# Optimization experiments

Measured on AMD Instinct MI355X. Metric: run time of the kernel, lower is better.

The kernel has to match this reference:

```python
import jax, jax.numpy as jnp
import numpy as np

B, L, D, N, KEEP, HID = 64, 256, 128, 8192, 64, 1024
IN_DIM = D + KEEP * D + 1  # q + packed subset keys + log_count


def setup_inputs() -> dict:
    key = jax.random.key(0)
    ks = jax.random.split(key, 7)
    q = jax.random.normal(ks[0], (N, D), jnp.float32)
    k = jax.random.normal(ks[1], (B, L, D), jnp.float32)
    batch_idx = jax.random.randint(ks[2], (N,), 0, B)
    mask = jax.random.randint(ks[3], (N, L), 0, 2).astype(bool)
    count = jax.random.randint(ks[4], (N,), 0, L)
    W1 = jax.random.normal(ks[5], (IN_DIM, HID), jnp.float32) / np.sqrt(IN_DIM).astype(np.float32)
    b1 = jnp.zeros((HID,), jnp.float32)
    W2 = jax.random.normal(ks[6], (HID, 1), jnp.float32) / np.sqrt(HID).astype(np.float32)
    b2 = jnp.zeros((1,), jnp.float32)
    return dict(q=q, k=k, batch_idx=batch_idx, mask=mask, count=count,
                W1=W1, b1=b1, W2=W2, b2=b2)


def _pack_subset_keys(k, batch_idx, mask):
    # chain_k: [N, L, D] gather of per-chain key blocks
    chain_k = k[batch_idx]
    pos = jnp.arange(L, dtype=jnp.float32)
    # score = L - pos for masked positions, 0 otherwise -> topk picks first KEEP masked positions
    scores = mask.astype(jnp.float32) * (jnp.float32(L) - pos)[None, :]
    top_scores, top_idx = jax.lax.top_k(scores, KEEP)
    picked = top_scores > 0
    sortable = jnp.where(picked, top_idx, L)  # sentinel L for unpicked
    sortable = jnp.sort(sortable, axis=1)     # restore ascending position order
    picked = sortable < L
    safe_idx = jnp.where(picked, sortable, 0)
    packed = jnp.take_along_axis(chain_k, safe_idx[:, :, None], axis=1)  # [N, KEEP, D]
    packed = packed * picked[:, :, None].astype(packed.dtype)
    return packed.reshape(N, KEEP * D)


def reference(q, k, batch_idx, mask, count, W1, b1, W2, b2):
    packed = _pack_subset_keys(k, batch_idx, mask)
    log_count = jnp.log1p(count.astype(q.dtype))[:, None]
    feat = jnp.concatenate([q, packed, log_count], axis=-1)  # [N, IN_DIM]
    h = jax.nn.gelu(feat @ W1 + b1, approximate=False)       # torch GELU = exact erf
    return (h @ W2 + b2).squeeze(-1)                          # [N]
```

## Files before the change

kernel.cpp:

```cpp
#include <hip/hip_runtime.h>
#include <math.h>

#define N_ROWS 8192
#define B_CH   64
#define L_SEQ  256
#define D_DIM  128
#define KEEP   64
#define HID    1024
#define KTOT   8320
#define KTILES 260
#define HTILES 64

#define KOFF   (N_ROWS * D_DIM)
#define ZOFF   (KOFF + B_CH * L_SEQ * D_DIM)
#define BUF_ELEMS (ZOFF + 128)

#define PACK_BLOCKS 256
#define QK_BLOCKS   1537
#define W1T_BLOCKS  2080
#define PREP_GRID   (PACK_BLOCKS + QK_BLOCKS + W1T_BLOCKS)

typedef unsigned short ushort_t;
typedef __attribute__((ext_vector_type(8))) short  short8;
typedef __attribute__((ext_vector_type(4))) float  float4v;

__device__ __forceinline__ ushort_t f2bf(float f) {
    union { float f; unsigned int u; } v; v.f = f;
    unsigned int u = v.u;
    unsigned int r = u + 0x7fffu + ((u >> 16) & 1u);
    return (ushort_t)(r >> 16);
}

__device__ __forceinline__ void glds16(const void* g, void* l) {
    __builtin_amdgcn_global_load_lds(
        (const __attribute__((address_space(1))) unsigned int*)g,
        (__attribute__((address_space(3))) unsigned int*)l,
        16, 0, 0);
}

__global__ void prep(const float* __restrict__ q, const float* __restrict__ k,
                     const float* __restrict__ W1, const int* __restrict__ mask,
                     const int* __restrict__ batch_idx, const int* __restrict__ count,
                     const float* __restrict__ b2,
                     ushort_t* __restrict__ buf, ushort_t* __restrict__ w1f,
                     int* __restrict__ srcLUT, float* __restrict__ logc,
                     float* __restrict__ out) {
    __shared__ __align__(16) char smem[16640];
    const int blk = blockIdx.x;
    const int t = threadIdx.x;

    if (blk < PACK_BLOCKS) {
        const int n0 = blk * 32;
        int* sidx = (int*)smem;
        int* bidx_l = (int*)(smem + 32 * 65 * 4);
        for (int i = t; i < 32 * 65; i += 256) sidx[i] = -1;
        if (t < 32) {
            int n = n0 + t;
            bidx_l[t] = batch_idx[n];
            logc[n] = log1pf((float)count[n]);
            srcLUT[n] = n * D_DIM;
            out[n] = b2[0];
        }
        __syncthreads();
        const int w = t >> 6, l = t & 63;
        const unsigned long long ltm = (1ull << l) - 1ull;
        for (int r = 0; r < 8; ++r) {
            const int lr = w * 8 + r;
            const int* mrow = mask + (size_t)(n0 + lr) * L_SEQ;
            int m0 = mrow[l] != 0;
            int m1 = mrow[64 + l] != 0;
            int m2 = mrow[128 + l] != 0;
            int m3 = mrow[192 + l] != 0;
            unsigned long long b0 = __ballot(m0), b1 = __ballot(m1);
            unsigned long long b2v = __ballot(m2), b3 = __ballot(m3);
            int p1 = (int)__popcll(b0);
            int p2 = p1 + (int)__popcll(b1);
            int p3 = p2 + (int)__popcll(b2v);
            int* row = sidx + lr * 65;
            if (m0) { int rk = (int)__popcll(b0 & ltm);       if (rk < KEEP) row[rk] = l; }
            if (m1) { int rk = p1 + (int)__popcll(b1 & ltm);  if (rk < KEEP) row[rk] = 64 + l; }
            if (m2) { int rk = p2 + (int)__popcll(b2v & ltm); if (rk < KEEP) row[rk] = 128 + l; }
            if (m3) { int rk = p3 + (int)__popcll(b3 & ltm);  if (rk < KEEP) row[rk] = 192 + l; }
        }
        __syncthreads();
        for (int e = t; e < KEEP * 32; e += 256) {
            int j = e >> 5, nl = e & 31;
            int s = sidx[nl * 65 + j];
            srcLUT[(size_t)(j + 1) * N_ROWS + n0 + nl] =
                (s >= 0) ? (KOFF + (bidx_l[nl] * L_SEQ + s) * D_DIM) : ZOFF;
        }

    } else if (blk < PACK_BLOCKS + QK_BLOCKS) {
        int c = (blk - PACK_BLOCKS) * 256 + t;
        if (c >= BUF_ELEMS / 8) return;
        int e = c * 8;
        float4 x0, x1;
        if (e < KOFF) {
            const float4* s = (const float4*)(q + e);
            x0 = s[0]; x1 = s[1];
        } else if (e < ZOFF) {
            const float4* s = (const float4*)(k + (e - KOFF));
            x0 = s[0]; x1 = s[1];
        } else {
            x0 = make_float4(0.f, 0.f, 0.f, 0.f);
            x1 = x0;
        }
        union { ushort_t s[8]; uint4 v; } o;
        o.s[0] = f2bf(x0.x); o.s[1] = f2bf(x0.y); o.s[2] = f2bf(x0.z); o.s[3] = f2bf(x0.w);
        o.s[4] = f2bf(x1.x); o.s[5] = f2bf(x1.y); o.s[6] = f2bf(x1.z); o.s[7] = f2bf(x1.w);
        *(uint4*)(buf + e) = o.v;

    } else {
        const int idx = blk - (PACK_BLOCKS + QK_BLOCKS);
        const int k0 = (idx % 130) * 64, h0 = (idx / 130) * 64;
        float (*tile)[65] = (float(*)[65])smem;
        const int hl = t & 63, kl = t >> 6;
#pragma unroll
        for (int i = 0; i < 16; ++i) {
            int kk = kl + i * 4;
            tile[kk][hl] = W1[(size_t)(k0 + kk) * HID + h0 + hl];
        }
        __syncthreads();
#pragma unroll
        for (int i = 0; i < 2; ++i) {
            int s = i * 256 + t;
            int c = s >> 6, l = s & 63;
            int qt = c >> 2, ht = c & 3;
            int ln = l & 15, quad = l >> 4;
            union { ushort_t sv[8]; uint4 v; } o;
#pragma unroll
            for (int j = 0; j < 8; ++j)
                o.sv[j] = f2bf(tile[qt * 32 + quad * 8 + j][ht * 16 + ln]);
            size_t dst = (((size_t)(h0 / 16 + ht) * KTILES + (k0 / 32 + qt)) * 64 + l) * 8;
            *(uint4*)(w1f + dst) = o.v;
        }
    }
}

__global__ __launch_bounds__(256, 2)
void gemm_mlp(const ushort_t* __restrict__ buf, const ushort_t* __restrict__ w1f,
              const int* __restrict__ srcLUT, const float* __restrict__ logc,
              const float* __restrict__ W1, const float* __restrict__ b1,
              const float* __restrict__ W2, float* __restrict__ out) {
    __shared__ ushort_t As[128 * 128];

    const int t = threadIdx.x;
    const int blkH = blockIdx.x, blkM = blockIdx.y;
    const int wave = t >> 6, lane = t & 63;
    const int wm = wave >> 1, wh = wave & 1;
    const int ln = lane & 15, quad = lane >> 4;

    float4v acc[4][4];
#pragma unroll
    for (int i = 0; i < 4; ++i)
#pragma unroll
        for (int j = 0; j < 4; ++j)
#pragma unroll
            for (int r = 0; r < 4; ++r) acc[i][j][r] = 0.0f;

    const int tr = t >> 4;
    const int pg = (t & 15) ^ tr;
    ushort_t* lA = As + t * 8;
    const int* lutBase = srcLUT + blkM * 128 + tr;

    const ushort_t* bp[4];
#pragma unroll
    for (int ni = 0; ni < 4; ++ni)
        bp[ni] = w1f + ((size_t)(blkH * 8 + wh * 4 + ni) * KTILES * 64 + lane) * 8;

    int offA[8];
#pragma unroll
    for (int i = 0; i < 8; ++i) offA[i] = lutBase[i * 16];

    for (int bi = 0; bi < 65; ++bi) {
#pragma unroll
        for (int i = 0; i < 8; ++i)
            glds16(buf + offA[i] + pg * 8, lA + i * 2048);
        short8 bq[4][4];
#pragma unroll
        for (int kk = 0; kk < 4; ++kk)
#pragma unroll
            for (int ni = 0; ni < 4; ++ni)
                bq[kk][ni] = *(const short8*)(bp[ni] + (size_t)(bi * 4 + kk) * 512);
        int offN[8];
        if (bi < 64) {
#pragma unroll
            for (int i = 0; i < 8; ++i) offN[i] = lutBase[(bi + 1) * N_ROWS + i * 16];
        }
        __syncthreads();
#pragma unroll
        for (int kk = 0; kk < 4; ++kk) {
            short8 af[4];
#pragma unroll
            for (int mi = 0; mi < 4; ++mi) {
                const int row = wm * 64 + mi * 16 + ln;
                const int sl = (kk * 4 + quad) ^ ln;
                af[mi] = *(const short8*)(As + row * 128 + sl * 8);
            }
#pragma unroll
            for (int mi = 0; mi < 4; ++mi)
#pragma unroll
                for (int ni = 0; ni < 4; ++ni)
                    acc[mi][ni] = __builtin_amdgcn_mfma_f32_16x16x32_bf16(
                        af[mi], bq[kk][ni], acc[mi][ni], 0, 0, 0);
        }
        __syncthreads();
#pragma unroll
        for (int i = 0; i < 8; ++i) offA[i] = offN[i];
    }

    const float* w1last = W1 + (size_t)KTOT * HID;
    float w1l[4], b1v[4], w2v[4];
#pragma unroll
    for (int ni = 0; ni < 4; ++ni) {
        int h = blkH * 128 + wh * 64 + ni * 16 + ln;
        w1l[ni] = w1last[h];
        b1v[ni] = b1[h];
        w2v[ni] = W2[h];
    }
    const int nbase = blkM * 128 + wm * 64 + quad * 4;
#pragma unroll
    for (int mi = 0; mi < 4; ++mi) {
#pragma unroll
        for (int rg = 0; rg < 4; ++rg) {
            const int n = nbase + mi * 16 + rg;
            const float lc = logc[n];
            float s = 0.0f;
#pragma unroll
            for (int ni = 0; ni < 4; ++ni) {
                float pre = acc[mi][ni][rg] + lc * w1l[ni] + b1v[ni];
                float hv = 0.5f * pre * (1.0f + erff(pre * 0.70710678118654752f));
                s += hv * w2v[ni];
            }
            s += __shfl_xor(s, 1);
            s += __shfl_xor(s, 2);
            s += __shfl_xor(s, 4);
            s += __shfl_xor(s, 8);
            if (ln == 0) atomicAdd(out + n, s);
        }
    }
}

extern "C" void kernel_launch(void* const* d_in, const int* in_sizes, int n_in,
                              void* d_out, int out_size, void* d_ws, size_t ws_size,
                              hipStream_t stream) {
    const float* q     = (const float*)d_in[0];
    const float* k     = (const float*)d_in[1];
    const int*   bidx  = (const int*)d_in[2];
    const int*   mask  = (const int*)d_in[3];
    const int*   count = (const int*)d_in[4];
    const float* W1    = (const float*)d_in[5];
    const float* b1    = (const float*)d_in[6];
    const float* W2    = (const float*)d_in[7];
    const float* b2    = (const float*)d_in[8];
    float* out = (float*)d_out;

    char* ws = (char*)d_ws;
    ushort_t* buf    = (ushort_t*)(ws);
    ushort_t* w1f    = (ushort_t*)(ws + 6291712);
    int*      srcLUT = (int*)(ws + 6291712 + 17039360);
    float*    logc   = (float*)(ws + 6291712 + 17039360 + 2129920);

    prep<<<PREP_GRID, 256, 0, stream>>>(q, k, W1, mask, bidx, count, b2,
                                        buf, w1f, srcLUT, logc, out);
    gemm_mlp<<<dim3(HID / 128, N_ROWS / 128), 256, 0, stream>>>(
        buf, w1f, srcLUT, logc, W1, b1, W2, out);
}
```

Baseline: 243.0 us.

## Double-buffer A tile in LDS and remap waves to 128x32 output strips

Shared memory for the A tile is doubled so the next K-slice's gathered rows and B fragments are loaded while the current slice is being multiplied, leaving one barrier per step instead of two. The wave layout also changes from 2x2 (64x64 each) to 4x1 along H (128 rows by 32 columns each). Each wave now reads twice as many A fragments from LDS per MFMA but fewer B fragments from global memory. LDS use doubles to 64KB per block and the B register buffers are duplicated, which may limit occupancy under launch_bounds(256,2).

```diff
diff --git a/kernel.cpp b/kernel.cpp
--- a/kernel.cpp
+++ b/kernel.cpp
@@ -9,7 +9,6 @@
 #define HID    1024
 #define KTOT   8320
 #define KTILES 260
-#define HTILES 64
 
 #define KOFF   (N_ROWS * D_DIM)
 #define ZOFF   (KOFF + B_CH * L_SEQ * D_DIM)
@@ -142,92 +141,112 @@
               const int* __restrict__ srcLUT, const float* __restrict__ logc,
               const float* __restrict__ W1, const float* __restrict__ b1,
               const float* __restrict__ W2, float* __restrict__ out) {
-    __shared__ ushort_t As[128 * 128];
+    __shared__ ushort_t As[2][128 * 128];
 
     const int t = threadIdx.x;
     const int blkH = blockIdx.x, blkM = blockIdx.y;
     const int wave = t >> 6, lane = t & 63;
-    const int wm = wave >> 1, wh = wave & 1;
     const int ln = lane & 15, quad = lane >> 4;
 
-    float4v acc[4][4];
-#pragma unroll
-    for (int i = 0; i < 4; ++i)
-#pragma unroll
-        for (int j = 0; j < 4; ++j)
+    float4v acc[8][2];
+#pragma unroll
+    for (int i = 0; i < 8; ++i)
+#pragma unroll
+        for (int j = 0; j < 2; ++j)
 #pragma unroll
             for (int r = 0; r < 4; ++r) acc[i][j][r] = 0.0f;
 
     const int tr = t >> 4;
     const int pg = (t & 15) ^ tr;
-    ushort_t* lA = As + t * 8;
     const int* lutBase = srcLUT + blkM * 128 + tr;
 
-    const ushort_t* bp[4];
-#pragma unroll
-    for (int ni = 0; ni < 4; ++ni)
-        bp[ni] = w1f + ((size_t)(blkH * 8 + wh * 4 + ni) * KTILES * 64 + lane) * 8;
-
-    int offA[8];
-#pragma unroll
-    for (int i = 0; i < 8; ++i) offA[i] = lutBase[i * 16];
-
-    for (int bi = 0; bi < 65; ++bi) {
+    const ushort_t* bp[2];
+#pragma unroll
+    for (int ni = 0; ni < 2; ++ni)
+        bp[ni] = w1f + ((size_t)(blkH * 8 + wave * 2 + ni) * KTILES * 64 + lane) * 8;
+
+    short8 bqA[4][2], bqB[4][2];
+    int offA[8], offB[8];
+
+#pragma unroll
+    for (int kk = 0; kk < 4; ++kk)
+#pragma unroll
+        for (int ni = 0; ni < 2; ++ni)
+            bqA[kk][ni] = *(const short8*)(bp[ni] + (size_t)kk * 512);
+    {
+        int off0[8];
+#pragma unroll
+        for (int i = 0; i < 8; ++i) off0[i] = lutBase[i * 16];
 #pragma unroll
         for (int i = 0; i < 8; ++i)
-            glds16(buf + offA[i] + pg * 8, lA + i * 2048);
-        short8 bq[4][4];
-#pragma unroll
-        for (int kk = 0; kk < 4; ++kk)
-#pragma unroll
-            for (int ni = 0; ni < 4; ++ni)
-                bq[kk][ni] = *(const short8*)(bp[ni] + (size_t)(bi * 4 + kk) * 512);
-        int offN[8];
-        if (bi < 64) {
-#pragma unroll
-            for (int i = 0; i < 8; ++i) offN[i] = lutBase[(bi + 1) * N_ROWS + i * 16];
-        }
-        __syncthreads();
-#pragma unroll
-        for (int kk = 0; kk < 4; ++kk) {
-            short8 af[4];
-#pragma unroll
-            for (int mi = 0; mi < 4; ++mi) {
-                const int row = wm * 64 + mi * 16 + ln;
-                const int sl = (kk * 4 + quad) ^ ln;
-                af[mi] = *(const short8*)(As + row * 128 + sl * 8);
-            }
-#pragma unroll
-            for (int mi = 0; mi < 4; ++mi)
-#pragma unroll
-                for (int ni = 0; ni < 4; ++ni)
-                    acc[mi][ni] = __builtin_amdgcn_mfma_f32_16x16x32_bf16(
-                        af[mi], bq[kk][ni], acc[mi][ni], 0, 0, 0);
-        }
-        __syncthreads();
-#pragma unroll
-        for (int i = 0; i < 8; ++i) offA[i] = offN[i];
-    }
+            glds16(buf + off0[i] + pg * 8, &As[0][(i * 256 + t) * 8]);
+    }
+#pragma unroll
+    for (int i = 0; i < 8; ++i) offA[i] = lutBase[N_ROWS + i * 16];
+
+#define GSTEP(bi, CUR, BQC, BQN, OFFC, OFFN)                                   \
+    {                                                                          \
+        __syncthreads();                                                       \
+        if ((bi) < 64) {                                                       \
+            _Pragma("unroll")                                                  \
+            for (int kk = 0; kk < 4; ++kk)                                     \
+                _Pragma("unroll")                                              \
+                for (int ni = 0; ni < 2; ++ni)                                 \
+                    BQN[kk][ni] = *(const short8*)(bp[ni] +                    \
+                        (size_t)(((bi) + 1) * 4 + kk) * 512);                  \
+            ushort_t* dA = &As[(CUR) ^ 1][0];                                  \
+            _Pragma("unroll")                                                  \
+            for (int i = 0; i < 8; ++i)                                        \
+                glds16(buf + OFFC[i] + pg * 8, dA + (i * 256 + t) * 8);        \
+            if ((bi) < 63) {                                                   \
+                _Pragma("unroll")                                              \
+                for (int i = 0; i < 8; ++i)                                    \
+                    OFFN[i] = lutBase[((bi) + 2) * N_ROWS + i * 16];           \
+            }                                                                  \
+        }                                                                      \
+        const ushort_t* rA = &As[CUR][0];                                      \
+        _Pragma("unroll")                                                      \
+        for (int kk = 0; kk < 4; ++kk) {                                       \
+            const int sl = (kk * 4 + quad) ^ ln;                               \
+            short8 af[8];                                                      \
+            _Pragma("unroll")                                                  \
+            for (int mi = 0; mi < 8; ++mi)                                     \
+                af[mi] = *(const short8*)(rA + (mi * 16 + ln) * 128 + sl * 8); \
+            _Pragma("unroll")                                                  \
+            for (int mi = 0; mi < 8; ++mi)                                     \
+                _Pragma("unroll")                                              \
+                for (int ni = 0; ni < 2; ++ni)                                 \
+                    acc[mi][ni] = __builtin_amdgcn_mfma_f32_16x16x32_bf16(     \
+                        af[mi], BQC[kk][ni], acc[mi][ni], 0, 0, 0);            \
+        }                                                                      \
+    }
+
+    for (int bi = 0; bi < 64; bi += 2) {
+        GSTEP(bi,     0, bqA, bqB, offA, offB);
+        GSTEP(bi + 1, 1, bqB, bqA, offB, offA);
+    }
+    GSTEP(64, 0, bqA, bqB, offA, offB);
+#undef GSTEP
 
     const float* w1last = W1 + (size_t)KTOT * HID;
-    float w1l[4], b1v[4], w2v[4];
-#pragma unroll
-    for (int ni = 0; ni < 4; ++ni) {
-        int h = blkH * 128 + wh * 64 + ni * 16 + ln;
+    float w1l[2], b1v[2], w2v[2];
+#pragma unroll
+    for (int ni = 0; ni < 2; ++ni) {
+        int h = blkH * 128 + wave * 32 + ni * 16 + ln;
         w1l[ni] = w1last[h];
         b1v[ni] = b1[h];
         w2v[ni] = W2[h];
     }
-    const int nbase = blkM * 128 + wm * 64 + quad * 4;
-#pragma unroll
-    for (int mi = 0; mi < 4; ++mi) {
+    const int nbase = blkM * 128 + quad * 4;
+#pragma unroll
+    for (int mi = 0; mi < 8; ++mi) {
 #pragma unroll
         for (int rg = 0; rg < 4; ++rg) {
             const int n = nbase + mi * 16 + rg;
             const float lc = logc[n];
             float s = 0.0f;
 #pragma unroll
-            for (int ni = 0; ni < 4; ++ni) {
+            for (int ni = 0; ni < 2; ++ni) {
                 float pre = acc[mi][ni][rg] + lc * w1l[ni] + b1v[ni];
                 float hv = 0.5f * pre * (1.0f + erff(pre * 0.70710678118654752f));
                 s += hv * w2v[ni];
```

New measurement: 264.7 us. 9.0% more time.
